# Optimization experiments

Measured on AMD Instinct MI355X. Metric: run time of the kernel, lower is better.

## Reference

```python
import jax, jax.numpy as jnp
import numpy as np

NUM_EXPERTS = 4
TOP_K = 2


def setup_inputs() -> dict:
    key = jax.random.key(0)
    ks = jax.random.split(key, 16)
    B, L, D, E, H = 8, 768, 1024, NUM_EXPERTS, 4096
    s = 0.02
    return {
        "context_c": jax.random.normal(ks[0], (B, L, D), jnp.float32),
        "time_cond": jax.random.normal(ks[1], (B, D), jnp.float32),
        "gate_w": jax.random.normal(ks[2], (3 * D, E), jnp.float32) * s,
        "gate_b": jnp.zeros((E,), jnp.float32),
        "time_w": jax.random.normal(ks[3], (D, 2 * E), jnp.float32) * s,
        "time_b": jnp.zeros((2 * E,), jnp.float32),
        "ew1": jax.random.normal(ks[4], (E, D, H), jnp.float32) * s,
        "eb1": jnp.zeros((E, H), jnp.float32),
        "ew2": jax.random.normal(ks[5], (E, H, D), jnp.float32) * s,
        "eb2": jnp.zeros((E, D), jnp.float32),
        "sw1": jax.random.normal(ks[6], (D, H), jnp.float32) * s,
        "sb1": jnp.zeros((H,), jnp.float32),
        "sw2": jax.random.normal(ks[7], (H, D), jnp.float32) * s,
        "sb2": jnp.zeros((D,), jnp.float32),
    }


def reference(context_c, time_cond, gate_w, gate_b, time_w, time_b,
              ew1, eb1, ew2, eb2, sw1, sb1, sw2, sb2):
    B, L, D = context_c.shape
    E, K = NUM_EXPERTS, TOP_K
    L_head = L_wrist = L // 3

    head = context_c[:, :L_head]                       # (B, Lh, D)
    wrist = context_c[:, L_head:L_head + L_wrist]      # (B, Lw, D)
    proprio = context_c[:, L_head + L_wrist:]          # (B, Lp, D)

    # modality-combination aggregates for the gate
    full_agg = context_c.mean(axis=1)
    hp_agg = jnp.concatenate([head, proprio], axis=1).mean(axis=1)
    wp_agg = jnp.concatenate([wrist, proprio], axis=1).mean(axis=1)
    gate_in = jnp.concatenate([full_agg, hp_agg, wp_agg], axis=-1)  # (B, 3D)

    gate_logits = gate_in @ gate_w + gate_b            # (B, E)
    mod = jax.nn.silu(time_cond) @ time_w + time_b     # (B, 2E)
    scale, shift = jnp.split(mod, 2, axis=-1)
    gate_logits = gate_logits * (1.0 + scale) + shift

    gate_scores = jax.nn.softmax(gate_logits, axis=-1)
    topk_w, topk_i = jax.lax.top_k(gate_scores, K)     # (B, K)
    topk_w = topk_w / (topk_w.sum(axis=-1, keepdims=True) + 1e-8)

    # per-sample combine weight per expert: (B, E)
    onehot = (topk_i[..., None] == jnp.arange(E)[None, None, :]).astype(context_c.dtype)
    w_be = jnp.sum(topk_w[..., None] * onehot, axis=1)

    # modality token masks per expert: expert 1 skips wrist, expert 2 skips head
    mask = np.ones((E, L), dtype=np.float32)
    mask[1, L_head:L_head + L_wrist] = 0.0
    mask[2, :L_head] = 0.0
    mask = jnp.asarray(mask)

    out = jnp.zeros_like(context_c)
    for e in range(E):  # small fixed expert loop; FFN is tokenwise so masking == routing
        h = jax.nn.gelu(context_c @ ew1[e] + eb1[e], approximate=True)
        y = h @ ew2[e] + eb2[e]                        # (B, L, D)
        out = out + (w_be[:, e][:, None, None] * mask[e][None, :, None]) * y

    shared = jax.nn.gelu(context_c @ sw1 + sb1, approximate=True) @ sw2 + sb2
    return out + shared
```

## Files before the change

### kernel.cpp

```cpp
#include <hip/hip_runtime.h>

using bf16x8 = __attribute__((ext_vector_type(8))) short;
using f32x4  = __attribute__((ext_vector_type(4))) float;
using u16x4  = __attribute__((ext_vector_type(4))) unsigned short;

#define AS1(p) ((__attribute__((address_space(1))) void*)(p))
#define AS3(p) ((__attribute__((address_space(3))) void*)(p))

template<int V> struct Ic { static constexpr int value = V; };

__device__ __forceinline__ unsigned short f2bf(float f){
  unsigned int x = __float_as_uint(f);
  unsigned int r = (x + 0x7FFFu + ((x >> 16) & 1u)) >> 16;
  return (unsigned short)r;
}
__device__ __forceinline__ float gelu_tanh(float x){
  float u = 0.7978845608028654f * (x + 0.044715f * x * x * x);
  float t = 1.f - 2.f / (__expf(2.f * u) + 1.f);
  return 0.5f * x * (1.f + t);
}

static constexpr int BB = 8, LL = 768, DD = 1024, HH = 4096, TT = 6144;

__global__ __launch_bounds__(256) void k0_transpose(const float* __restrict__ srcE,
                                                    const float* __restrict__ srcS,
                                                    unsigned short* __restrict__ dst,
                                                    int R, int C){
  __shared__ float tile[64][65];
  int z = blockIdx.z;
  const float* src = (z < 4) ? srcE + (size_t)z * R * C : srcS;
  unsigned short* d = dst + (size_t)z * R * C;
  int c0 = blockIdx.x * 64, r0 = blockIdx.y * 64;
  int tx = threadIdx.x & 15, ty = threadIdx.x >> 4;
  #pragma unroll
  for (int rep = 0; rep < 4; rep++){
    int r = ty + rep * 16;
    float4 v = *(const float4*)(src + (size_t)(r0 + r) * C + c0 + tx * 4);
    tile[r][tx * 4 + 0] = v.x; tile[r][tx * 4 + 1] = v.y;
    tile[r][tx * 4 + 2] = v.z; tile[r][tx * 4 + 3] = v.w;
  }
  __syncthreads();
  #pragma unroll
  for (int rep = 0; rep < 4; rep++){
    int c = ty + rep * 16;
    u16x4 o;
    o[0] = f2bf(tile[tx * 4 + 0][c]); o[1] = f2bf(tile[tx * 4 + 1][c]);
    o[2] = f2bf(tile[tx * 4 + 2][c]); o[3] = f2bf(tile[tx * 4 + 3][c]);
    *(u16x4*)(d + (size_t)(c0 + c) * R + r0 + tx * 4) = o;
  }
}

__global__ __launch_bounds__(256) void k1x_cvt_partial(const float* __restrict__ X,
                                                       unsigned short* __restrict__ Xb,
                                                       float* __restrict__ part){
  int ch = blockIdx.x, b = blockIdx.y, t = threadIdx.x;
  size_t rowbase = ((size_t)(b * LL + ch * 32)) * DD;
  const float4* src = (const float4*)(X + rowbase);
  u16x4* dst = (u16x4*)(Xb + rowbase);
  float4 s; s.x = s.y = s.z = s.w = 0.f;
  for (int l = 0; l < 32; l++){
    float4 v = src[l * 256 + t];
    u16x4 o;
    o[0] = f2bf(v.x); o[1] = f2bf(v.y); o[2] = f2bf(v.z); o[3] = f2bf(v.w);
    dst[l * 256 + t] = o;
    s.x += v.x; s.y += v.y; s.z += v.z; s.w += v.w;
  }
  ((float4*)(part + ((size_t)(b * 24 + ch)) * DD))[t] = s;
}

__global__ __launch_bounds__(256) void k1b_gate(const float* __restrict__ part,
                                                const float* __restrict__ tc,
                                                const float* __restrict__ gw,
                                                const float* __restrict__ gb,
                                                const float* __restrict__ tw,
                                                const float* __restrict__ tb,
                                                float* __restrict__ wtop, int* __restrict__ itop){
  int b = blockIdx.x, t = threadIdx.x;
  __shared__ float glog[4], gmod[8];
  if (t < 4) glog[t] = 0.f;
  if (t < 8) gmod[t] = 0.f;
  __syncthreads();
  float lacc[4] = {0.f,0.f,0.f,0.f};
  float macc[8] = {0.f,0.f,0.f,0.f,0.f,0.f,0.f,0.f};
  for (int dd = 0; dd < 4; dd++){
    int d = dd * 256 + t;
    const float* pb = part + (size_t)b * 24 * DD + d;
    float sh = 0.f, sw = 0.f, sp = 0.f;
    for (int c2 = 0; c2 < 8; c2++){
      sh += pb[(0  + c2) * DD];
      sw += pb[(8  + c2) * DD];
      sp += pb[(16 + c2) * DD];
    }
    float fa = (sh + sw + sp) * (1.f / 768.f);
    float hp = (sh + sp) * (1.f / 512.f);
    float wp = (sw + sp) * (1.f / 512.f);
    #pragma unroll
    for (int e = 0; e < 4; e++){
      lacc[e] += fa * gw[(size_t)d * 4 + e]
               + hp * gw[(size_t)(DD + d) * 4 + e]
               + wp * gw[(size_t)(2 * DD + d) * 4 + e];
    }
    float v = tc[(size_t)b * DD + d];
    float sl = v / (1.f + __expf(-v));
    #pragma unroll
    for (int j = 0; j < 8; j++) macc[j] += sl * tw[(size_t)d * 8 + j];
  }
  #pragma unroll
  for (int e = 0; e < 4; e++) atomicAdd(&glog[e], lacc[e]);
  #pragma unroll
  for (int j = 0; j < 8; j++) atomicAdd(&gmod[j], macc[j]);
  __syncthreads();
  if (t == 0){
    float lg[4];
    #pragma unroll
    for (int e = 0; e < 4; e++){
      float sc = gmod[e]     + tb[e];
      float sf = gmod[4 + e] + tb[4 + e];
      lg[e] = (glog[e] + gb[e]) * (1.f + sc) + sf;
    }
    float mx = fmaxf(fmaxf(lg[0], lg[1]), fmaxf(lg[2], lg[3]));
    float p[4], s = 0.f;
    #pragma unroll
    for (int e = 0; e < 4; e++){ p[e] = __expf(lg[e] - mx); s += p[e]; }
    #pragma unroll
    for (int e = 0; e < 4; e++) p[e] /= s;
    int i0 = 0;
    for (int e = 1; e < 4; e++) if (p[e] > p[i0]) i0 = e;
    int i1 = (i0 == 0) ? 1 : 0;
    for (int e = 0; e < 4; e++) if (e != i0 && p[e] > p[i1]) i1 = e;
    float den = p[i0] + p[i1] + 1e-8f;
    wtop[b * 2 + 0] = p[i0] / den;  wtop[b * 2 + 1] = p[i1] / den;
    itop[b * 2 + 0] = i0;           itop[b * 2 + 1] = i1;
  }
}

#define MMA_Q(AF, BQ, MH, NH)                                                   \
  {                                                                             \
    _Pragma("unroll") for (int ks = 0; ks < 2; ks++)                            \
    _Pragma("unroll") for (int mf = 0; mf < 4; mf++)                            \
    _Pragma("unroll") for (int nf = 0; nf < 2; nf++)                            \
      acc[(MH)*4+mf][(NH)*2+nf] = __builtin_amdgcn_mfma_f32_16x16x32_bf16(      \
          (AF)[mf][ks], (BQ)[nf][ks], acc[(MH)*4+mf][(NH)*2+nf], 0, 0, 0);      \
  }

__device__ __forceinline__ void gemm256_core(const unsigned short* __restrict__ A,
                                             const unsigned short* __restrict__ B,
                                             int lda, int ldb, int nkt,
                                             unsigned short* ldsA,
                                             unsigned short* ldsB,
                                             f32x4 (&acc)[8][4]){
  const int t = threadIdx.x;
  const int lane = t & 63, quad = lane >> 4, r = lane & 15;
  const int wave = t >> 6, wm = wave >> 2, wn = wave & 3;
  const int welem = (t & 448) * 8;

  int offA[2], offB[2];
  #pragma unroll
  for (int j = 0; j < 2; j++){
    int x = t * 16 + j * 8192;
    int y = x ^ (((x >> 7) & 7) << 4);
    int cr = y >> 7, kel = (y & 127) >> 1;
    offA[j] = (((cr >> 6) << 7) + (cr & 63)) * lda + kel;
    offB[j] = (((cr >> 5) << 6) + (cr & 31)) * ldb + kel;
  }
  const int ldam = 64 * lda, ldbn = 32 * ldb;

  auto stA = [&](int buf, int mh, int kt){
    #pragma unroll
    for (int j = 0; j < 2; j++)
      __builtin_amdgcn_global_load_lds(AS1(A + offA[j] + mh * ldam + kt * 64),
          AS3(ldsA + (buf * 2 + mh) * 8192 + welem + j * 4096), 16, 0, 0);
  };
  auto stB = [&](int buf, int nh, int kt){
    #pragma unroll
    for (int j = 0; j < 2; j++)
      __builtin_amdgcn_global_load_lds(AS1(B + offB[j] + nh * ldbn + kt * 64),
          AS3(ldsB + (buf * 2 + nh) * 8192 + welem + j * 4096), 16, 0, 0);
  };
  auto ldA = [&](int buf, int mh, bf16x8 (&dst)[4][2]){
    #pragma unroll
    for (int mf = 0; mf < 4; mf++){
      int cr = wm * 64 + mf * 16 + r;
      const unsigned short* p = ldsA + (buf * 2 + mh) * 8192 + cr * 64;
      int sw = (cr & 7) << 3;
      dst[mf][0] = *(const bf16x8*)(p + ((quad * 8) ^ sw));
      dst[mf][1] = *(const bf16x8*)(p + ((32 + quad * 8) ^ sw));
    }
  };
  auto ldB = [&](int buf, int nh, bf16x8 (&dst)[2][2]){
    #pragma unroll
    for (int nf = 0; nf < 2; nf++){
      int cc = wn * 32 + nf * 16 + r;
      const unsigned short* p = ldsB + (buf * 2 + nh) * 8192 + cc * 64;
      int sw = (cc & 7) << 3;
      dst[nf][0] = *(const bf16x8*)(p + ((quad * 8) ^ sw));
      dst[nf][1] = *(const bf16x8*)(p + ((32 + quad * 8) ^ sw));
    }
  };

  auto ktile = [&](auto bufc, int kt, bool pf1, bool pf2){
    constexpr int BUF = decltype(bufc)::value;
    bf16x8 af[4][2], b0[2][2], b1[2][2];
    ldA(BUF, 0, af); ldB(BUF, 0, b0);
    if (pf1) stA(BUF ^ 1, 1, kt + 1);
    __builtin_amdgcn_s_barrier();
    __builtin_amdgcn_s_setprio(1);
    MMA_Q(af, b0, 0, 0);
    __builtin_amdgcn_s_setprio(0);
    __builtin_amdgcn_s_barrier();
    ldB(BUF, 1, b1);
    if (pf2) stA(BUF, 0, kt + 2);
    __builtin_amdgcn_s_barrier();
    __builtin_amdgcn_s_setprio(1);
    MMA_Q(af, b1, 0, 1);
    __builtin_amdgcn_s_setprio(0);
    __builtin_amdgcn_s_barrier();
    ldA(BUF, 1, af);
    if (pf2) stB(BUF, 0, kt + 2);
    __builtin_amdgcn_s_barrier();
    __builtin_amdgcn_s_setprio(1);
    MMA_Q(af, b1, 1, 1);
    __builtin_amdgcn_s_setprio(0);
    __builtin_amdgcn_s_barrier();
    if (pf2) stB(BUF, 1, kt + 2);
    __builtin_amdgcn_s_barrier();
    __builtin_amdgcn_s_setprio(1);
    MMA_Q(af, b0, 1, 0);
    __builtin_amdgcn_s_setprio(0);
    if (pf1){
      if (pf2) asm volatile("s_waitcnt vmcnt(6)" ::: "memory");
      else     asm volatile("s_waitcnt vmcnt(0)" ::: "memory");
    }
    __builtin_amdgcn_s_barrier();
  };

  stA(0, 0, 0); stB(0, 0, 0); stB(0, 1, 0); stA(0, 1, 0);
  stA(1, 0, 1); stB(1, 0, 1); stB(1, 1, 1);
  asm volatile("s_waitcnt vmcnt(6)" ::: "memory");
  __builtin_amdgcn_s_barrier();

  int kt = 0;
  for (; kt + 2 < nkt; kt += 2){
    ktile(Ic<0>{}, kt,     true, true);
    ktile(Ic<1>{}, kt + 1, true, true);
  }
  ktile(Ic<0>{}, nkt - 2, true,  false);
  ktile(Ic<1>{}, nkt - 1, false, false);
}

__device__ __forceinline__ void mask_weight(int e, int seg, float& w){
  if ((e == 1 && seg == 1) || (e == 2 && seg == 0)) w = 0.f;
}

template<int GX, int GY>
__device__ __forceinline__ void xcd_swizzle(int& bx, int& by, int& bz){
  int lin = blockIdx.x + GX * (blockIdx.y + GY * blockIdx.z);
  int nwg = GX * GY * gridDim.z;
  int q = nwg >> 3;
  int swz = (lin & 7) * q + (lin >> 3);
  bx = swz % GX; int rem = swz / GX; by = rem % GY; bz = rem / GY;
}

__global__ __launch_bounds__(512, 2) void k2_gemm1(const unsigned short* __restrict__ Xb,
                                                   const unsigned short* __restrict__ w1t,
                                                   const float* __restrict__ eb1,
                                                   const float* __restrict__ sb1,
                                                   const float* __restrict__ wtop,
                                                   const int* __restrict__ itop,
                                                   unsigned short* __restrict__ Hws){
  int bx, by, bz; xcd_swizzle<24, 16>(bx, by, bz);
  int m0 = bx * 256, n0 = by * 256, slot = bz;
  int b = m0 / LL, seg = (m0 % LL) / 256;
  int mat; float w;
  if (slot == 0){ mat = 4; w = 1.f; }
  else {
    int k = slot - 1;
    mat = itop[b * 2 + k];
    w = wtop[b * 2 + k];
    mask_weight(mat, seg, w);
    if (w == 0.f) return;
  }
  __shared__ __align__(16) unsigned short ldsA[32768];
  __shared__ __align__(16) unsigned short ldsB[32768];
  f32x4 acc[8][4];
  #pragma unroll
  for (int mi = 0; mi < 8; mi++)
    #pragma unroll
    for (int ni = 0; ni < 4; ni++)
      #pragma unroll
      for (int c = 0; c < 4; c++) acc[mi][ni][c] = 0.f;

  gemm256_core(Xb + (size_t)m0 * DD,
               w1t + (size_t)mat * HH * DD + (size_t)n0 * DD,
               DD, DD, DD / 64, ldsA, ldsB, acc);

  int t = threadIdx.x, lane = t & 63, wave = t >> 6;
  int quad = lane >> 4, r = lane & 15, wm = wave >> 2, wn = wave & 3;
  const float* b1 = (mat == 4) ? sb1 : eb1 + (size_t)mat * HH;
  unsigned short* Hout = Hws + (size_t)slot * TT * HH;
  #pragma unroll
  for (int ni = 0; ni < 4; ni++){
    int col = n0 + wn * 64 + ni * 16 + r;
    float bias = b1[col];
    #pragma unroll
    for (int mi = 0; mi < 8; mi++){
      #pragma unroll
      for (int r2 = 0; r2 < 4; r2++){
        int row = m0 + wm * 128 + mi * 16 + quad * 4 + r2;
        Hout[(size_t)row * HH + col] = f2bf(gelu_tanh(acc[mi][ni][r2] + bias) * w);
      }
    }
  }
}

__global__ __launch_bounds__(512, 2) void k3a_gemm2(const unsigned short* __restrict__ Hws,
                                                    const unsigned short* __restrict__ w2t,
                                                    const float* __restrict__ eb2,
                                                    const float* __restrict__ sb2,
                                                    const float* __restrict__ wtop,
                                                    const int* __restrict__ itop,
                                                    float* __restrict__ out,
                                                    float* __restrict__ p1){
  int bx, by, bz; xcd_swizzle<24, 4>(bx, by, bz);
  int m0 = bx * 256, n0 = by * 256, kh = bz;
  int b = m0 / LL, seg = (m0 % LL) / 256;
  __shared__ __align__(16) unsigned short ldsA[32768];
  __shared__ __align__(16) unsigned short ldsB[32768];
  f32x4 acc[8][4];
  #pragma unroll
  for (int mi = 0; mi < 8; mi++)
    #pragma unroll
    for (int ni = 0; ni < 4; ni++)
      #pragma unroll
      for (int c = 0; c < 4; c++) acc[mi][ni][c] = 0.f;

  int emat[2]; float ew[2];
  #pragma unroll
  for (int k = 0; k < 2; k++){
    emat[k] = itop[b * 2 + k];
    ew[k] = wtop[b * 2 + k];
    mask_weight(emat[k], seg, ew[k]);
  }
  for (int slot = 0; slot < 3; slot++){
    int mat;
    if (slot == 0) mat = 4;
    else { if (ew[slot - 1] == 0.f) continue; mat = emat[slot - 1]; }
    gemm256_core(Hws + (size_t)slot * TT * HH + (size_t)m0 * HH + kh * 2048,
                 w2t + (size_t)mat * DD * HH + (size_t)n0 * HH + kh * 2048,
                 HH, HH, 2048 / 64, ldsA, ldsB, acc);
  }
  int t = threadIdx.x, lane = t & 63, wave = t >> 6;
  int quad = lane >> 4, r = lane & 15, wm = wave >> 2, wn = wave & 3;
  if (kh == 0){
    #pragma unroll
    for (int ni = 0; ni < 4; ni++){
      int col = n0 + wn * 64 + ni * 16 + r;
      float bias = sb2[col];
      if (ew[0] > 0.f) bias += ew[0] * eb2[(size_t)emat[0] * DD + col];
      if (ew[1] > 0.f) bias += ew[1] * eb2[(size_t)emat[1] * DD + col];
      #pragma unroll
      for (int mi = 0; mi < 8; mi++)
        #pragma unroll
        for (int r2 = 0; r2 < 4; r2++){
          int row = m0 + wm * 128 + mi * 16 + quad * 4 + r2;
          out[(size_t)row * DD + col] = acc[mi][ni][r2] + bias;
        }
    }
  } else {
    #pragma unroll
    for (int ni = 0; ni < 4; ni++){
      int col = n0 + wn * 64 + ni * 16 + r;
      #pragma unroll
      for (int mi = 0; mi < 8; mi++)
        #pragma unroll
        for (int r2 = 0; r2 < 4; r2++){
          int row = m0 + wm * 128 + mi * 16 + quad * 4 + r2;
          p1[(size_t)row * DD + col] = acc[mi][ni][r2];
        }
    }
  }
}

__global__ __launch_bounds__(256) void k3r_reduce(float* __restrict__ out,
                                                  const float* __restrict__ p1){
  size_t i = (size_t)blockIdx.x * 256 + threadIdx.x;
  float4 a = ((const float4*)out)[i];
  float4 b = ((const float4*)p1)[i];
  a.x += b.x; a.y += b.y; a.z += b.z; a.w += b.w;
  ((float4*)out)[i] = a;
}

extern "C" void kernel_launch(void* const* d_in, const int* in_sizes, int n_in,
                              void* d_out, int out_size, void* d_ws, size_t ws_size,
                              hipStream_t stream){
  const float* X   = (const float*)d_in[0];
  const float* tc  = (const float*)d_in[1];
  const float* gw  = (const float*)d_in[2];
  const float* gb  = (const float*)d_in[3];
  const float* tw  = (const float*)d_in[4];
  const float* tb  = (const float*)d_in[5];
  const float* ew1 = (const float*)d_in[6];
  const float* eb1 = (const float*)d_in[7];
  const float* ew2 = (const float*)d_in[8];
  const float* eb2 = (const float*)d_in[9];
  const float* sw1 = (const float*)d_in[10];
  const float* sb1 = (const float*)d_in[11];
  const float* sw2 = (const float*)d_in[12];
  const float* sb2 = (const float*)d_in[13];
  float* out = (float*)d_out;
  char* ws = (char*)d_ws;

  const size_t off_part = 0;
  const size_t off_wtop = 786432;
  const size_t off_itop = 786560;
  const size_t off_xb   = 1ull << 20;
  const size_t off_w1t  = 14ull << 20;
  const size_t off_w2t  = off_w1t + 41943040ull;
  const size_t off_h    = off_w2t + 41943040ull;
  const size_t need     = off_h + 150994944ull;
  if (ws_size < need) return;

  float* part = (float*)(ws + off_part);
  float* wtop = (float*)(ws + off_wtop);
  int*   itop = (int*)(ws + off_itop);
  unsigned short* Xb  = (unsigned short*)(ws + off_xb);
  unsigned short* w1t = (unsigned short*)(ws + off_w1t);
  unsigned short* w2t = (unsigned short*)(ws + off_w2t);
  unsigned short* Hws = (unsigned short*)(ws + off_h);
  float* p1 = (float*)(ws + off_w1t);

  k1x_cvt_partial<<<dim3(24, 8), 256, 0, stream>>>(X, Xb, part);
  k0_transpose<<<dim3(64, 16, 5), 256, 0, stream>>>(ew1, sw1, w1t, 1024, 4096);
  k0_transpose<<<dim3(16, 64, 5), 256, 0, stream>>>(ew2, sw2, w2t, 4096, 1024);
  k1b_gate<<<dim3(8), 256, 0, stream>>>(part, tc, gw, gb, tw, tb, wtop, itop);
  k2_gemm1<<<dim3(24, 16, 3), 512, 0, stream>>>(Xb, w1t, eb1, sb1, wtop, itop, Hws);
  k3a_gemm2<<<dim3(24, 4, 2), 512, 0, stream>>>(Hws, w2t, eb2, sb2, wtop, itop, out, p1);
  k3r_reduce<<<dim3(6144), 256, 0, stream>>>(out, p1);
}
```

Measured before the change: 643.2 us.

## Stage GEMM1 epilogue through LDS for vectorized stores; drop XCD swizzle

The GEMM1 epilogue now writes the GELU-scaled bf16 tile into shared memory, then copies it out with 16-byte row-contiguous stores instead of scattered 2-byte global stores. The aim is better write coalescing for the large hidden-activation buffer. Separately, the XCD-aware block-index swizzle is removed from both GEMM kernels and plain block indices are used, which may change L2 locality across XCDs. The LDS round trip adds barriers and likely bank conflicts on the strided element writes.

```diff
diff --git a/kernel.cpp b/kernel.cpp
--- a/kernel.cpp
+++ b/kernel.cpp
@@ -3,6 +3,7 @@
 using bf16x8 = __attribute__((ext_vector_type(8))) short;
 using f32x4  = __attribute__((ext_vector_type(4))) float;
 using u16x4  = __attribute__((ext_vector_type(4))) unsigned short;
+using u16x8  = __attribute__((ext_vector_type(8))) unsigned short;
 
 #define AS1(p) ((__attribute__((address_space(1))) void*)(p))
 #define AS3(p) ((__attribute__((address_space(3))) void*)(p))
@@ -252,15 +253,6 @@
   if ((e == 1 && seg == 1) || (e == 2 && seg == 0)) w = 0.f;
 }
 
-template<int GX, int GY>
-__device__ __forceinline__ void xcd_swizzle(int& bx, int& by, int& bz){
-  int lin = blockIdx.x + GX * (blockIdx.y + GY * blockIdx.z);
-  int nwg = GX * GY * gridDim.z;
-  int q = nwg >> 3;
-  int swz = (lin & 7) * q + (lin >> 3);
-  bx = swz % GX; int rem = swz / GX; by = rem % GY; bz = rem / GY;
-}
-
 __global__ __launch_bounds__(512, 2) void k2_gemm1(const unsigned short* __restrict__ Xb,
                                                    const unsigned short* __restrict__ w1t,
                                                    const float* __restrict__ eb1,
@@ -268,8 +260,7 @@
                                                    const float* __restrict__ wtop,
                                                    const int* __restrict__ itop,
                                                    unsigned short* __restrict__ Hws){
-  int bx, by, bz; xcd_swizzle<24, 16>(bx, by, bz);
-  int m0 = bx * 256, n0 = by * 256, slot = bz;
+  int m0 = blockIdx.x * 256, n0 = blockIdx.y * 256, slot = blockIdx.z;
   int b = m0 / LL, seg = (m0 % LL) / 256;
   int mat; float w;
   if (slot == 0){ mat = 4; w = 1.f; }
@@ -280,8 +271,9 @@
     mask_weight(mat, seg, w);
     if (w == 0.f) return;
   }
-  __shared__ __align__(16) unsigned short ldsA[32768];
-  __shared__ __align__(16) unsigned short ldsB[32768];
+  __shared__ __align__(16) unsigned short lds[65536];
+  unsigned short* ldsA = lds;
+  unsigned short* ldsB = lds + 32768;
   f32x4 acc[8][4];
   #pragma unroll
   for (int mi = 0; mi < 8; mi++)
@@ -298,18 +290,27 @@
   int quad = lane >> 4, r = lane & 15, wm = wave >> 2, wn = wave & 3;
   const float* b1 = (mat == 4) ? sb1 : eb1 + (size_t)mat * HH;
   unsigned short* Hout = Hws + (size_t)slot * TT * HH;
+  __syncthreads();
   #pragma unroll
   for (int ni = 0; ni < 4; ni++){
-    int col = n0 + wn * 64 + ni * 16 + r;
-    float bias = b1[col];
+    int col = wn * 64 + ni * 16 + r;
+    float bias = b1[n0 + col];
     #pragma unroll
     for (int mi = 0; mi < 8; mi++){
       #pragma unroll
       for (int r2 = 0; r2 < 4; r2++){
-        int row = m0 + wm * 128 + mi * 16 + quad * 4 + r2;
-        Hout[(size_t)row * HH + col] = f2bf(gelu_tanh(acc[mi][ni][r2] + bias) * w);
+        int row = wm * 128 + mi * 16 + quad * 4 + r2;
+        lds[row * 256 + col] = f2bf(gelu_tanh(acc[mi][ni][r2] + bias) * w);
       }
     }
+  }
+  __syncthreads();
+  #pragma unroll
+  for (int it = 0; it < 16; it++){
+    int chunk = it * 512 + t;
+    int row = chunk >> 5, sg = chunk & 31;
+    u16x8 v = *(const u16x8*)(lds + row * 256 + sg * 8);
+    *(u16x8*)(Hout + (size_t)(m0 + row) * HH + n0 + sg * 8) = v;
   }
 }
 
@@ -321,8 +322,7 @@
                                                     const int* __restrict__ itop,
                                                     float* __restrict__ out,
                                                     float* __restrict__ p1){
-  int bx, by, bz; xcd_swizzle<24, 4>(bx, by, bz);
-  int m0 = bx * 256, n0 = by * 256, kh = bz;
+  int m0 = blockIdx.x * 256, n0 = blockIdx.y * 256, kh = blockIdx.z;
   int b = m0 / LL, seg = (m0 % LL) / 256;
   __shared__ __align__(16) unsigned short ldsA[32768];
   __shared__ __align__(16) unsigned short ldsB[32768];
```

Measured after the change: 625.5 us. 1.03x faster.
